# Kernel tuning notes

Hardware: AMD Instinct MI355X
Metric: run time of the kernel (lower is better)

Reference implementation:

```python
import jax, jax.numpy as jnp
import numpy as np

D_KEY = 128
INF = 1e9  # stands in for the module's global INF constant


def setup_inputs() -> dict:
    key = jax.random.key(0)
    kq, kk, kv = jax.random.split(key, 3)
    B, S, D = 8, 4096, D_KEY
    return {
        "query": jax.random.normal(kq, (B, S, D), dtype=jnp.float32),
        "keys": jax.random.normal(kk, (B, S, D), dtype=jnp.float32),
        "values": jax.random.normal(kv, (B, S, D), dtype=jnp.float32),
    }


def reference(query, keys, values):
    # dot_products: [B, Sq, Sk]
    scores = jnp.einsum("bqd,bkd->bqk", query, keys)
    S = scores.shape[-1]
    # causal: subtract INF on strict upper triangle (triu(1)), applied BEFORE scaling
    causal = jnp.triu(jnp.ones((S, S), dtype=scores.dtype), 1) * INF
    logits = (scores - causal[None, :, :]) / jnp.asarray(np.sqrt(D_KEY), scores.dtype)
    # legacy F.softmax on 3D transposed tensor == softmax over key axis
    probs = jax.nn.softmax(logits, axis=-1)
    # dropout with p=0.0 is identity
    return jnp.einsum("bqk,bkd->bqd", probs, values)
```

## Files before the change

### kernel.cpp

```cpp
#include <hip/hip_runtime.h>
#include <hip/hip_bf16.h>

#define B_SZ   8
#define S_LEN  4096
#define D_K    128
#define KB     64
#define CH     16
#define NCHUNK 1280

#define KT_STR 136
#define VT_STR 72
#define PT_STR 72

typedef short  short8  __attribute__((ext_vector_type(8)));
typedef float  floatx4 __attribute__((ext_vector_type(4)));

#define EXP2F(x) exp2f(x)

__device__ __forceinline__ unsigned bfround(float x) {
  unsigned u = __builtin_bit_cast(unsigned, x);
  return (u + 0x7fffu + ((u >> 16) & 1u)) >> 16;
}
__device__ __forceinline__ unsigned bfpack2(float a, float b) {
  return bfround(a) | (bfround(b) << 16);
}


__global__ __launch_bounds__(256)
void conv_k(const float* __restrict__ K, unsigned short* __restrict__ Kb) {
  const size_t idx = ((size_t)blockIdx.x * 256 + threadIdx.x) * 8;
  float4 f0 = *(const float4*)(K + idx);
  float4 f1 = *(const float4*)(K + idx + 4);
  uint4 u;
  u.x = bfpack2(f0.x, f0.y);
  u.y = bfpack2(f0.z, f0.w);
  u.z = bfpack2(f1.x, f1.y);
  u.w = bfpack2(f1.z, f1.w);
  *(uint4*)(Kb + idx) = u;
}

__global__ __launch_bounds__(256)
void transp_v(const float* __restrict__ V, unsigned short* __restrict__ Vt) {
  __shared__ float tile[64][65];
  const int t   = threadIdx.x;
  const int bid = blockIdx.x;
  const int b   = bid >> 7;
  const int rem = bid & 127;
  const int kt  = (rem >> 1) * 64;
  const int dt  = (rem & 1) * 64;
  {
    const int c  = (t & 15) * 4;
    const int r0 = t >> 4;
#pragma unroll
    for (int rr = 0; rr < 4; ++rr) {
      const int r = r0 + rr * 16;
      float4 f = *(const float4*)(V + (size_t)(b * S_LEN + kt + r) * D_K + dt + c);
      tile[r][c]     = f.x;
      tile[r][c + 1] = f.y;
      tile[r][c + 2] = f.z;
      tile[r][c + 3] = f.w;
    }
  }
  __syncthreads();
  {
    const int d  = t >> 2;
    const int k0 = (t & 3) * 16;
#pragma unroll
    for (int j = 0; j < 16; j += 8) {
      uint4 u;
      u.x = bfpack2(tile[k0 + j + 0][d], tile[k0 + j + 1][d]);
      u.y = bfpack2(tile[k0 + j + 2][d], tile[k0 + j + 3][d]);
      u.z = bfpack2(tile[k0 + j + 4][d], tile[k0 + j + 5][d]);
      u.w = bfpack2(tile[k0 + j + 6][d], tile[k0 + j + 7][d]);
      *(uint4*)(Vt + (size_t)(b * D_K + dt + d) * S_LEN + kt + k0 + j) = u;
    }
  }
}

__global__ void zero_cnt(int* cnt) { *cnt = 0; }


__global__ __launch_bounds__(128, 2)
void attn_worker(const float* __restrict__ Q, const unsigned short* __restrict__ Kb,
                 const unsigned short* __restrict__ Vt, int* __restrict__ cnt,
                 float* __restrict__ ml, float* __restrict__ pO) {
  __shared__ __align__(16) short Klds[KB * KT_STR];
  __shared__ __align__(16) short Vtlds[D_K * VT_STR];
  __shared__ __align__(16) short Plds[2 * 16 * PT_STR];
  __shared__ int s_chunk;

  const int tid  = threadIdx.x;
  const int lane = tid & 63;
  const int w    = tid >> 6;
  const int l15  = lane & 15;
  const int quad = lane >> 4;

  const int kr0 = tid >> 4;
  const int kc  = (tid & 15) * 8;
  const int vr0 = tid >> 3;
  const int vc  = (tid & 7) * 8;

  const float CSC = 0.12752041f;

  for (;;) {
    if (tid == 0) s_chunk = atomicAdd(cnt, 1);
    __syncthreads();
    const int c = s_chunk;
    if (c >= NCHUNK) break;

    int b, qi, j;
    if (c < 800) {
      const int r = c >> 3;  b = c & 7;
      if      (r <  4) { qi = 63;               j = r;            }
      else if (r < 52) { qi = 62 - (r-4)/3;     j = (r-4)%3;      }
      else if (r < 84) { qi = 46 - (r-52)/2;    j = (r-52)%2;     }
      else             { qi = 30 - (r-84);      j = 0;            }
    } else {
      const int rc = c - 800;
      const int s  = 15 - (rc >> 5);
      const int t  = rc & 31;
      b  = t & 7;
      qi = s - 1 + 16 * (t >> 3);
      j  = (qi + 1) >> 4;
    }

    const int q0 = qi * 64;
    const int s0 = j * CH;
    const int s1 = min(s0 + CH, qi + 1);

    short8 bq[2][4];
    int qg[2];
#pragma unroll
    for (int sub = 0; sub < 2; ++sub) {
      qg[sub] = q0 + w * 32 + sub * 16 + l15;
      const float* qrow = Q + (size_t)(b * S_LEN + qg[sub]) * D_K + quad * 8;
#pragma unroll
      for (int kd = 0; kd < 4; ++kd) {
        float4 f0 = *(const float4*)(qrow + kd * 32);
        float4 f1 = *(const float4*)(qrow + kd * 32 + 4);
        union { short8 s; unsigned u[4]; } t;
        t.u[0] = bfpack2(f0.x, f0.y);
        t.u[1] = bfpack2(f0.z, f0.w);
        t.u[2] = bfpack2(f1.x, f1.y);
        t.u[3] = bfpack2(f1.z, f1.w);
        bq[sub][kd] = t.s;
      }
    }

    floatx4 acc[2][8];
#pragma unroll
    for (int sub = 0; sub < 2; ++sub)
#pragma unroll
      for (int nc = 0; nc < 8; ++nc) acc[sub][nc] = (floatx4){0.f, 0.f, 0.f, 0.f};
    float m_run[2] = {-1e30f, -1e30f}, l_run[2] = {0.f, 0.f};

    const unsigned short* kbase = Kb + (size_t)(b * S_LEN) * D_K;
    const unsigned short* vbase = Vt + (size_t)(b * D_K) * S_LEN;

    for (int s = s0; s < s1; ++s) {
      const int kt = s * KB;

#pragma unroll
      for (int i = 0; i < 8; ++i) {
        uint4 u = *(const uint4*)(kbase + (size_t)(kt + kr0 + i * 8) * D_K + kc);
        *(uint4*)(&Klds[(kr0 + i * 8) * KT_STR + kc]) = u;
      }
#pragma unroll
      for (int i = 0; i < 8; ++i) {
        uint4 u = *(const uint4*)(vbase + (size_t)(vr0 + i * 16) * S_LEN + kt + vc);
        *(uint4*)(&Vtlds[(vr0 + i * 16) * VT_STR + vc]) = u;
      }
      __syncthreads();

      floatx4 st[2][4];
#pragma unroll
      for (int kf = 0; kf < 4; ++kf) {
        floatx4 c0 = (floatx4){0.f, 0.f, 0.f, 0.f};
        floatx4 c1 = (floatx4){0.f, 0.f, 0.f, 0.f};
#pragma unroll
        for (int kd = 0; kd < 4; ++kd) {
          short8 a = *(const short8*)(&Klds[(kf * 16 + l15) * KT_STR + kd * 32 + quad * 8]);
          c0 = __builtin_amdgcn_mfma_f32_16x16x32_bf16(a, bq[0][kd], c0, 0, 0, 0);
          c1 = __builtin_amdgcn_mfma_f32_16x16x32_bf16(a, bq[1][kd], c1, 0, 0, 0);
        }
        st[0][kf] = c0;
        st[1][kf] = c1;
      }

      if (s == qi) {
#pragma unroll
        for (int sub = 0; sub < 2; ++sub)
#pragma unroll
          for (int kf = 0; kf < 4; ++kf)
#pragma unroll
            for (int r = 0; r < 4; ++r) {
              int key = kt + kf * 16 + quad * 4 + r;
              if (key > qg[sub]) st[sub][kf][r] = -1e30f;
            }
      }

      short8 pa[2][2];
#pragma unroll
      for (int sub = 0; sub < 2; ++sub) {
        float mx = st[sub][0][0];
#pragma unroll
        for (int kf = 0; kf < 4; ++kf)
#pragma unroll
          for (int r = 0; r < 4; ++r) mx = fmaxf(mx, st[sub][kf][r]);
        mx = fmaxf(mx, __shfl_xor(mx, 16, 64));
        mx = fmaxf(mx, __shfl_xor(mx, 32, 64));
        const float m_new = fmaxf(m_run[sub], mx);
        const float alpha = EXP2F((m_run[sub] - m_new) * CSC);

        float p[4][4];
        float tsum = 0.f;
#pragma unroll
        for (int kf = 0; kf < 4; ++kf)
#pragma unroll
          for (int r = 0; r < 4; ++r) {
            p[kf][r] = EXP2F((st[sub][kf][r] - m_new) * CSC);
            tsum += p[kf][r];
          }
        tsum += __shfl_xor(tsum, 16, 64);
        tsum += __shfl_xor(tsum, 32, 64);
        l_run[sub] = l_run[sub] * alpha + tsum;
        m_run[sub] = m_new;

#pragma unroll
        for (int r = 0; r < 4; ++r) {
          const float ar = __shfl(alpha, quad * 4 + r, 64);
#pragma unroll
          for (int nc = 0; nc < 8; ++nc) acc[sub][nc][r] *= ar;
        }

        short* pw = &Plds[(w * 16 + l15) * PT_STR];
#pragma unroll
        for (int kf = 0; kf < 4; ++kf) {
          uint2 u;
          u.x = bfpack2(p[kf][0], p[kf][1]);
          u.y = bfpack2(p[kf][2], p[kf][3]);
          *(uint2*)(&pw[kf * 16 + quad * 4]) = u;
        }
        __asm__ __volatile__("" ::: "memory");
        pa[sub][0] = *(const short8*)(&pw[quad * 8]);
        pa[sub][1] = *(const short8*)(&pw[32 + quad * 8]);
        __asm__ __volatile__("" ::: "memory");
      }

#pragma unroll
      for (int nc = 0; nc < 8; ++nc) {
        short8 bv0 = *(const short8*)(&Vtlds[(nc * 16 + l15) * VT_STR + quad * 8]);
        short8 bv1 = *(const short8*)(&Vtlds[(nc * 16 + l15) * VT_STR + 32 + quad * 8]);
        acc[0][nc] = __builtin_amdgcn_mfma_f32_16x16x32_bf16(pa[0][0], bv0, acc[0][nc], 0, 0, 0);
        acc[0][nc] = __builtin_amdgcn_mfma_f32_16x16x32_bf16(pa[0][1], bv1, acc[0][nc], 0, 0, 0);
        acc[1][nc] = __builtin_amdgcn_mfma_f32_16x16x32_bf16(pa[1][0], bv0, acc[1][nc], 0, 0, 0);
        acc[1][nc] = __builtin_amdgcn_mfma_f32_16x16x32_bf16(pa[1][1], bv1, acc[1][nc], 0, 0, 0);
      }
      __syncthreads();
    }

    const int slot = ((b << 6) | qi) * 4 + j;
    float* po = pO + (size_t)slot * 8192;
#pragma unroll
    for (int sub = 0; sub < 2; ++sub) {
#pragma unroll
      for (int r = 0; r < 4; ++r) {
        const int qrow = w * 32 + sub * 16 + quad * 4 + r;
        float* op = po + qrow * D_K + l15;
#pragma unroll
        for (int nc = 0; nc < 8; ++nc) op[nc * 16] = acc[sub][nc][r];
      }
      if (quad == 0) {
        const int qrow = w * 32 + sub * 16 + l15;
        ml[(size_t)slot * 128 + qrow * 2]     = m_run[sub];
        ml[(size_t)slot * 128 + qrow * 2 + 1] = l_run[sub];
      }
    }
  }
}


__global__ __launch_bounds__(256)
void attn_combine(const float* __restrict__ ml, const float* __restrict__ pO,
                  float* __restrict__ O) {
  const int t   = blockIdx.x;
  const int b   = t >> 6;
  const int qi  = t & 63;
  const int ncb = ((qi + 1) + 15) >> 4;
  const float CSC = 0.12752041f;

  const int tid = threadIdx.x;
  const int q   = tid >> 2;
  const int dp  = (tid & 3) * 32;

  float m[4], l[4];
  float M = -1e30f;
  for (int jj = 0; jj < ncb; ++jj) {
    const int slot = t * 4 + jj;
    m[jj] = ml[(size_t)slot * 128 + q * 2];
    l[jj] = ml[(size_t)slot * 128 + q * 2 + 1];
    M = fmaxf(M, m[jj]);
  }
  float wgt[4], L = 0.f;
  for (int jj = 0; jj < ncb; ++jj) {
    wgt[jj] = EXP2F((m[jj] - M) * CSC);
    L += wgt[jj] * l[jj];
  }
  const float inv = 1.0f / L;

  float4 out[8];
#pragma unroll
  for (int v = 0; v < 8; ++v) out[v] = make_float4(0.f, 0.f, 0.f, 0.f);
  for (int jj = 0; jj < ncb; ++jj) {
    const float* src = pO + (size_t)(t * 4 + jj) * 8192 + q * D_K + dp;
    const float wj = wgt[jj];
#pragma unroll
    for (int v = 0; v < 8; ++v) {
      float4 f = *(const float4*)(src + v * 4);
      out[v].x += wj * f.x;  out[v].y += wj * f.y;
      out[v].z += wj * f.z;  out[v].w += wj * f.w;
    }
  }
  float* dst = O + (size_t)(b * S_LEN + qi * 64 + q) * D_K + dp;
#pragma unroll
  for (int v = 0; v < 8; ++v) {
    float4 f = make_float4(out[v].x * inv, out[v].y * inv, out[v].z * inv, out[v].w * inv);
    *(float4*)(dst + v * 4) = f;
  }
}


__global__ __launch_bounds__(256, 2)
void attn_fwd_fb(const float* __restrict__ Q, const float* __restrict__ K,
                 const float* __restrict__ V, float* __restrict__ O) {
  __shared__ __align__(16) short Klds[KB * KT_STR];
  __shared__ __align__(16) short Vtlds[D_K * VT_STR];
  __shared__ __align__(16) short Plds[4 * 16 * PT_STR];

  const int tid  = threadIdx.x;
  const int lane = tid & 63;
  const int w    = tid >> 6;
  const int l15  = lane & 15;
  const int quad = lane >> 4;

  const int bid = blockIdx.x;
  const int b   = bid & 7;
  const int qi  = 63 - (bid >> 3);
  const int q0  = qi * 64;

  const float CSC = 0.12752041f;

  const int    qg   = q0 + w * 16 + l15;
  const float* qrow = Q + (size_t)(b * S_LEN + qg) * D_K + quad * 8;
  short8 bq[4];
#pragma unroll
  for (int kd = 0; kd < 4; ++kd) {
    float4 f0 = *(const float4*)(qrow + kd * 32);
    float4 f1 = *(const float4*)(qrow + kd * 32 + 4);
    union { short8 s; unsigned u[4]; } t;
    t.u[0] = bfpack2(f0.x, f0.y);
    t.u[1] = bfpack2(f0.z, f0.w);
    t.u[2] = bfpack2(f1.x, f1.y);
    t.u[3] = bfpack2(f1.z, f1.w);
    bq[kd] = t.s;
  }

  floatx4 acc[8];
#pragma unroll
  for (int nc = 0; nc < 8; ++nc) acc[nc] = (floatx4){0.f, 0.f, 0.f, 0.f};
  float m_run = -1e30f, l_run = 0.f;

  const int d4 = tid & 31;
  const int kq = tid >> 5;
  const int nsteps = qi + 1;

  for (int s = 0; s < nsteps; ++s) {
    const int kt = s * KB;
#pragma unroll
    for (int r2 = 0; r2 < 2; ++r2) {
      const int row = r2 * 32 + kq * 4;
      const float* kp = K + (size_t)(b * S_LEN + kt + row) * D_K + d4 * 4;
      const float* vp = V + (size_t)(b * S_LEN + kt + row) * D_K + d4 * 4;
      float4 fk[4], fv[4];
#pragma unroll
      for (int i = 0; i < 4; ++i) {
        fk[i] = *(const float4*)(kp + i * D_K);
        fv[i] = *(const float4*)(vp + i * D_K);
      }
#pragma unroll
      for (int i = 0; i < 4; ++i) {
        uint2 u;
        u.x = bfpack2(fk[i].x, fk[i].y);
        u.y = bfpack2(fk[i].z, fk[i].w);
        *(uint2*)(&Klds[(row + i) * KT_STR + d4 * 4]) = u;
      }
#pragma unroll
      for (int c = 0; c < 4; ++c) {
        float e0 = ((const float*)&fv[0])[c];
        float e1 = ((const float*)&fv[1])[c];
        float e2 = ((const float*)&fv[2])[c];
        float e3 = ((const float*)&fv[3])[c];
        uint2 u;
        u.x = bfpack2(e0, e1);
        u.y = bfpack2(e2, e3);
        *(uint2*)(&Vtlds[(d4 * 4 + c) * VT_STR + row]) = u;
      }
    }
    __syncthreads();

    floatx4 st[4];
#pragma unroll
    for (int kf = 0; kf < 4; ++kf) {
      floatx4 c = (floatx4){0.f, 0.f, 0.f, 0.f};
#pragma unroll
      for (int kd = 0; kd < 4; ++kd) {
        short8 a = *(const short8*)(&Klds[(kf * 16 + l15) * KT_STR + kd * 32 + quad * 8]);
        c = __builtin_amdgcn_mfma_f32_16x16x32_bf16(a, bq[kd], c, 0, 0, 0);
      }
      st[kf] = c;
    }

    if (s == nsteps - 1) {
#pragma unroll
      for (int kf = 0; kf < 4; ++kf)
#pragma unroll
        for (int r = 0; r < 4; ++r) {
          int key = kt + kf * 16 + quad * 4 + r;
          if (key > qg) st[kf][r] = -1e30f;
        }
    }

    float mx = st[0][0];
#pragma unroll
    for (int kf = 0; kf < 4; ++kf)
#pragma unroll
      for (int r = 0; r < 4; ++r) mx = fmaxf(mx, st[kf][r]);
    mx = fmaxf(mx, __shfl_xor(mx, 16, 64));
    mx = fmaxf(mx, __shfl_xor(mx, 32, 64));
    const float m_new = fmaxf(m_run, mx);
    const float alpha = EXP2F((m_run - m_new) * CSC);

    float p[4][4];
    float tsum = 0.f;
#pragma unroll
    for (int kf = 0; kf < 4; ++kf)
#pragma unroll
      for (int r = 0; r < 4; ++r) {
        p[kf][r] = EXP2F((st[kf][r] - m_new) * CSC);
        tsum += p[kf][r];
      }
    tsum += __shfl_xor(tsum, 16, 64);
    tsum += __shfl_xor(tsum, 32, 64);
    l_run = l_run * alpha + tsum;
    m_run = m_new;

#pragma unroll
    for (int r = 0; r < 4; ++r) {
      const float ar = __shfl(alpha, quad * 4 + r, 64);
#pragma unroll
      for (int nc = 0; nc < 8; ++nc) acc[nc][r] *= ar;
    }

    short* pw = &Plds[(w * 16 + l15) * PT_STR];
#pragma unroll
    for (int kf = 0; kf < 4; ++kf) {
      uint2 u;
      u.x = bfpack2(p[kf][0], p[kf][1]);
      u.y = bfpack2(p[kf][2], p[kf][3]);
      *(uint2*)(&pw[kf * 16 + quad * 4]) = u;
    }
    __asm__ __volatile__("" ::: "memory");
    short8 pa0 = *(const short8*)(&pw[quad * 8]);
    short8 pa1 = *(const short8*)(&pw[32 + quad * 8]);

#pragma unroll
    for (int nc = 0; nc < 8; ++nc) {
      short8 bv0 = *(const short8*)(&Vtlds[(nc * 16 + l15) * VT_STR + quad * 8]);
      acc[nc] = __builtin_amdgcn_mfma_f32_16x16x32_bf16(pa0, bv0, acc[nc], 0, 0, 0);
      short8 bv1 = *(const short8*)(&Vtlds[(nc * 16 + l15) * VT_STR + 32 + quad * 8]);
      acc[nc] = __builtin_amdgcn_mfma_f32_16x16x32_bf16(pa1, bv1, acc[nc], 0, 0, 0);
    }
    __syncthreads();
  }

#pragma unroll
  for (int r = 0; r < 4; ++r) {
    const float lr  = __shfl(l_run, quad * 4 + r, 64);
    const float inv = 1.0f / lr;
    const int qout  = q0 + w * 16 + quad * 4 + r;
    float* op = O + (size_t)(b * S_LEN + qout) * D_K + l15;
#pragma unroll
    for (int nc = 0; nc < 8; ++nc) op[nc * 16] = acc[nc][r] * inv;
  }
}


extern "C" void kernel_launch(void* const* d_in, const int* in_sizes, int n_in,
                              void* d_out, int out_size, void* d_ws, size_t ws_size,
                              hipStream_t stream) {
  const float* Q = (const float*)d_in[0];
  const float* K = (const float*)d_in[1];
  const float* V = (const float*)d_in[2];
  float* O = (float*)d_out;

  const size_t elems = (size_t)B_SZ * S_LEN * D_K;

  const size_t off_ml = 256;
  const size_t off_po = off_ml + 2048ull * 128 * 4;
  const size_t off_kb = off_po + 2048ull * 8192 * 4;
  const size_t off_vt = off_kb + elems * 2;
  const size_t need   = off_vt + elems * 2;

  if (ws_size >= need) {
    char* ws = (char*)d_ws;
    int*            cnt = (int*)ws;
    float*          ml  = (float*)(ws + off_ml);
    float*          po  = (float*)(ws + off_po);
    unsigned short* Kb  = (unsigned short*)(ws + off_kb);
    unsigned short* Vt  = (unsigned short*)(ws + off_vt);

    zero_cnt<<<dim3(1), dim3(1), 0, stream>>>(cnt);
    conv_k<<<dim3((unsigned)(elems / 8 / 256)), dim3(256), 0, stream>>>(K, Kb);
    transp_v<<<dim3(B_SZ * (S_LEN / 64) * (D_K / 64)), dim3(256), 0, stream>>>(V, Vt);
    attn_worker<<<dim3(1024), dim3(128), 0, stream>>>(Q, Kb, Vt, cnt, ml, po);
    attn_combine<<<dim3(512), dim3(256), 0, stream>>>(ml, po, O);
  } else {
    attn_fwd_fb<<<dim3(512), dim3(256), 0, stream>>>(Q, K, V, O);
  }
}
```

Before: 195.3 us.

## Double-buffer K/V tiles via async global-to-LDS DMA with pre-swizzled tile layout

Merges the K conversion and V transpose into one prep kernel that writes each 64-key tile as a contiguous 8192-element block, with an XOR swizzle matching the LDS read pattern. The attention worker now double-buffers K and V tiles in LDS using global_load_lds DMA, prefetching tile s+2 while tile s is computed. This is meant to hide global-load latency and avoid bank conflicts without padded strides. P packing also switches to the hardware v_cvt_pk_bf16_f32 instruction. The cost is doubled LDS use, which may limit occupancy, plus hand-managed waitcnt/barrier ordering that is fragile.

After: 217.7 us. 1.11x slower.

```diff
diff --git a/kernel.cpp b/kernel.cpp
--- a/kernel.cpp
+++ b/kernel.cpp
@@ -1,5 +1,4 @@
 #include <hip/hip_runtime.h>
-#include <hip/hip_bf16.h>
 
 #define B_SZ   8
 #define S_LEN  4096
@@ -8,8 +7,6 @@
 #define CH     16
 #define NCHUNK 1280
 
-#define KT_STR 136
-#define VT_STR 72
 #define PT_STR 72
 
 typedef short  short8  __attribute__((ext_vector_type(8)));
@@ -24,55 +21,80 @@
 __device__ __forceinline__ unsigned bfpack2(float a, float b) {
   return bfround(a) | (bfround(b) << 16);
 }
+__device__ __forceinline__ unsigned cvtpk(float lo, float hi) {
+  unsigned r;
+  asm("v_cvt_pk_bf16_f32 %0, %1, %2" : "=v"(r) : "v"(lo), "v"(hi));
+  return r;
+}
+
+__device__ __forceinline__ void dma16(const void* g, const void* l) {
+  __builtin_amdgcn_global_load_lds(
+      (__attribute__((address_space(1))) unsigned int*)(unsigned long long)g,
+      (__attribute__((address_space(3))) unsigned int*)(unsigned int)(unsigned long long)l,
+      16, 0, 0);
+}
 
 
 __global__ __launch_bounds__(256)
-void conv_k(const float* __restrict__ K, unsigned short* __restrict__ Kb) {
-  const size_t idx = ((size_t)blockIdx.x * 256 + threadIdx.x) * 8;
-  float4 f0 = *(const float4*)(K + idx);
-  float4 f1 = *(const float4*)(K + idx + 4);
-  uint4 u;
-  u.x = bfpack2(f0.x, f0.y);
-  u.y = bfpack2(f0.z, f0.w);
-  u.z = bfpack2(f1.x, f1.y);
-  u.w = bfpack2(f1.z, f1.w);
-  *(uint4*)(Kb + idx) = u;
-}
-
-__global__ __launch_bounds__(256)
-void transp_v(const float* __restrict__ V, unsigned short* __restrict__ Vt) {
-  __shared__ float tile[64][65];
-  const int t   = threadIdx.x;
+void prep(const float* __restrict__ K, const float* __restrict__ V,
+          unsigned short* __restrict__ Kb, unsigned short* __restrict__ Vt) {
+  __shared__ float tile[64][129];
+  const int tid = threadIdx.x;
   const int bid = blockIdx.x;
-  const int b   = bid >> 7;
-  const int rem = bid & 127;
-  const int kt  = (rem >> 1) * 64;
-  const int dt  = (rem & 1) * 64;
+  const int b   = bid >> 6;
+  const int s   = bid & 63;
+  const int kt  = s * 64;
+
   {
-    const int c  = (t & 15) * 4;
-    const int r0 = t >> 4;
-#pragma unroll
-    for (int rr = 0; rr < 4; ++rr) {
-      const int r = r0 + rr * 16;
-      float4 f = *(const float4*)(V + (size_t)(b * S_LEN + kt + r) * D_K + dt + c);
-      tile[r][c]     = f.x;
-      tile[r][c + 1] = f.y;
-      tile[r][c + 2] = f.z;
-      tile[r][c + 3] = f.w;
+    const int r  = tid >> 2;
+    const int cq = tid & 3;
+    const float* kp = K + (size_t)(b * S_LEN + kt + r) * D_K + cq * 32;
+    unsigned short* kdst = Kb + (size_t)bid * 8192 + r * 128;
+    const int xr = (r & 7) << 4;
+#pragma unroll
+    for (int j = 0; j < 4; ++j) {
+      float4 f0 = *(const float4*)(kp + j * 8);
+      float4 f1 = *(const float4*)(kp + j * 8 + 4);
+      uint4 u;
+      u.x = bfpack2(f0.x, f0.y);
+      u.y = bfpack2(f0.z, f0.w);
+      u.z = bfpack2(f1.x, f1.y);
+      u.w = bfpack2(f1.z, f1.w);
+      const int o = (cq * 64 + j * 16) ^ xr;
+      *(uint4*)(kdst + (o >> 1)) = u;
+    }
+  }
+
+  {
+    const int k  = tid >> 2;
+    const int cq = tid & 3;
+    const float* vp = V + (size_t)(b * S_LEN + kt + k) * D_K + cq * 32;
+#pragma unroll
+    for (int i = 0; i < 8; ++i) {
+      float4 f = *(const float4*)(vp + i * 4);
+      tile[k][cq * 32 + i * 4]     = f.x;
+      tile[k][cq * 32 + i * 4 + 1] = f.y;
+      tile[k][cq * 32 + i * 4 + 2] = f.z;
+      tile[k][cq * 32 + i * 4 + 3] = f.w;
     }
   }
   __syncthreads();
+
   {
-    const int d  = t >> 2;
-    const int k0 = (t & 3) * 16;
-#pragma unroll
-    for (int j = 0; j < 16; j += 8) {
+    const int d = tid >> 1;
+    const int h = tid & 1;
+    unsigned short* vdst = Vt + (size_t)bid * 8192 + d * 64;
+    const int xr = (d & 7) << 4;
+#pragma unroll
+    for (int j = 0; j < 4; ++j) {
+      const int k0 = h * 32 + j * 8;
       uint4 u;
-      u.x = bfpack2(tile[k0 + j + 0][d], tile[k0 + j + 1][d]);
-      u.y = bfpack2(tile[k0 + j + 2][d], tile[k0 + j + 3][d]);
-      u.z = bfpack2(tile[k0 + j + 4][d], tile[k0 + j + 5][d]);
-      u.w = bfpack2(tile[k0 + j + 6][d], tile[k0 + j + 7][d]);
-      *(uint4*)(Vt + (size_t)(b * D_K + dt + d) * S_LEN + kt + k0 + j) = u;
+      u.x = bfpack2(tile[k0 + 0][d], tile[k0 + 1][d]);
+      u.y = bfpack2(tile[k0 + 2][d], tile[k0 + 3][d]);
+      u.z = bfpack2(tile[k0 + 4][d], tile[k0 + 5][d]);
+      u.w = bfpack2(tile[k0 + 6][d], tile[k0 + 7][d]);
+      const int o = (h * 64 + j * 16) ^ xr;
+      *(uint4*)(vdst + (o >> 1)) = u;
     }
   }
 }
@@ -84,8 +106,8 @@
 void attn_worker(const float* __restrict__ Q, const unsigned short* __restrict__ Kb,
                  const unsigned short* __restrict__ Vt, int* __restrict__ cnt,
                  float* __restrict__ ml, float* __restrict__ pO) {
-  __shared__ __align__(16) short Klds[KB * KT_STR];
-  __shared__ __align__(16) short Vtlds[D_K * VT_STR];
+  __shared__ __align__(16) short Klds[2][8192];
+  __shared__ __align__(16) short Vtlds[2][8192];
   __shared__ __align__(16) short Plds[2 * 16 * PT_STR];
   __shared__ int s_chunk;
 
@@ -94,11 +116,7 @@
   const int w    = tid >> 6;
   const int l15  = lane & 15;
   const int quad = lane >> 4;
-
-  const int kr0 = tid >> 4;
-  const int kc  = (tid & 15) * 8;
-  const int vr0 = tid >> 3;
-  const int vc  = (tid & 7) * 8;
+  const int xk   = (l15 & 7) << 3;
 
   const float CSC = 0.12752041f;
 
@@ -154,23 +172,37 @@
       for (int nc = 0; nc < 8; ++nc) acc[sub][nc] = (floatx4){0.f, 0.f, 0.f, 0.f};
     float m_run[2] = {-1e30f, -1e30f}, l_run[2] = {0.f, 0.f};
 
-    const unsigned short* kbase = Kb + (size_t)(b * S_LEN) * D_K;
-    const unsigned short* vbase = Vt + (size_t)(b * D_K) * S_LEN;
+    const unsigned short* kb0 = Kb + (size_t)b * 64 * 8192;
+    const unsigned short* vb0 = Vt + (size_t)b * 64 * 8192;
+    const int lo = lane * 8;
+
+#define STAGE(BUF, S)                                                          \
+    do {                                                                       \
+      const unsigned short* kg_ = kb0 + (size_t)(S) * 8192 + w * 4096 + lo;    \
+      const unsigned short* vg_ = vb0 + (size_t)(S) * 8192 + w * 4096 + lo;    \
+      short* kl_ = &Klds[BUF][w * 4096];                                       \
+      short* vl_ = &Vtlds[BUF][w * 4096];                                      \
+      _Pragma("unroll")                                                        \
+      for (int i_ = 0; i_ < 8; ++i_) dma16(kg_ + i_ * 512, kl_ + i_ * 512);    \
+      _Pragma("unroll")                                                        \
+      for (int i_ = 0; i_ < 8; ++i_) dma16(vg_ + i_ * 512, vl_ + i_ * 512);    \
+    } while (0)
+
+    STAGE(s0 & 1, s0);
+    if (s0 + 1 < s1) {
+      STAGE((s0 + 1) & 1, s0 + 1);
+      asm volatile("s_waitcnt vmcnt(16)" ::: "memory");
+    } else {
+      asm volatile("s_waitcnt vmcnt(0)" ::: "memory");
+    }
+    __builtin_amdgcn_s_barrier();
+    __builtin_amdgcn_sched_barrier(0);
 
     for (int s = s0; s < s1; ++s) {
-      const int kt = s * KB;
-
-#pragma unroll
-      for (int i = 0; i < 8; ++i) {
-        uint4 u = *(const uint4*)(kbase + (size_t)(kt + kr0 + i * 8) * D_K + kc);
-        *(uint4*)(&Klds[(kr0 + i * 8) * KT_STR + kc]) = u;
-      }
-#pragma unroll
-      for (int i = 0; i < 8; ++i) {
-        uint4 u = *(const uint4*)(vbase + (size_t)(vr0 + i * 16) * S_LEN + kt + vc);
-        *(uint4*)(&Vtlds[(vr0 + i * 16) * VT_STR + vc]) = u;
-      }
-      __syncthreads();
+      const int kt  = s * KB;
+      const int cur = s & 1;
+      const short* Kl = &Klds[cur][0];
+      const short* Vl = &Vtlds[cur][0];
 
       floatx4 st[2][4];
 #pragma unroll
@@ -179,7 +211,7 @@
         floatx4 c1 = (floatx4){0.f, 0.f, 0.f, 0.f};
 #pragma unroll
         for (int kd = 0; kd < 4; ++kd) {
-          short8 a = *(const short8*)(&Klds[(kf * 16 + l15) * KT_STR + kd * 32 + quad * 8]);
+          short8 a = *(const short8*)(&Kl[((kf * 16 + l15) << 7) + ((kd * 32 + quad * 8) ^ xk)]);
           c0 = __builtin_amdgcn_mfma_f32_16x16x32_bf16(a, bq[0][kd], c0, 0, 0, 0);
           c1 = __builtin_amdgcn_mfma_f32_16x16x32_bf16(a, bq[1][kd], c1, 0, 0, 0);
         }
@@ -237,8 +269,8 @@
 #pragma unroll
         for (int kf = 0; kf < 4; ++kf) {
           uint2 u;
-          u.x = bfpack2(p[kf][0], p[kf][1]);
-          u.y = bfpack2(p[kf][2], p[kf][3]);
+          u.x = cvtpk(p[kf][0], p[kf][1]);
+          u.y = cvtpk(p[kf][2], p[kf][3]);
           *(uint2*)(&pw[kf * 16 + quad * 4]) = u;
         }
         __asm__ __volatile__("" ::: "memory");
@@ -249,15 +281,27 @@
 
 #pragma unroll
       for (int nc = 0; nc < 8; ++nc) {
-        short8 bv0 = *(const short8*)(&Vtlds[(nc * 16 + l15) * VT_STR + quad * 8]);
-        short8 bv1 = *(const short8*)(&Vtlds[(nc * 16 + l15) * VT_STR + 32 + quad * 8]);
+        short8 bv0 = *(const short8*)(&Vl[((nc * 16 + l15) << 6) + ((quad * 8) ^ xk)]);
+        short8 bv1 = *(const short8*)(&Vl[((nc * 16 + l15) << 6) + ((32 + quad * 8) ^ xk)]);
         acc[0][nc] = __builtin_amdgcn_mfma_f32_16x16x32_bf16(pa[0][0], bv0, acc[0][nc], 0, 0, 0);
         acc[0][nc] = __builtin_amdgcn_mfma_f32_16x16x32_bf16(pa[0][1], bv1, acc[0][nc], 0, 0, 0);
         acc[1][nc] = __builtin_amdgcn_mfma_f32_16x16x32_bf16(pa[1][0], bv0, acc[1][nc], 0, 0, 0);
         acc[1][nc] = __builtin_amdgcn_mfma_f32_16x16x32_bf16(pa[1][1], bv1, acc[1][nc], 0, 0, 0);
       }
-      __syncthreads();
-    }
+
+      asm volatile("s_waitcnt lgkmcnt(0)" ::: "memory");
+      __builtin_amdgcn_s_barrier();
+      __builtin_amdgcn_sched_barrier(0);
+      if (s + 2 < s1) {
+        STAGE(cur, s + 2);
+        asm volatile("s_waitcnt vmcnt(16)" ::: "memory");
+      } else if (s + 1 < s1) {
+        asm volatile("s_waitcnt vmcnt(0)" ::: "memory");
+      }
+      __builtin_amdgcn_s_barrier();
+      __builtin_amdgcn_sched_barrier(0);
+    }
+#undef STAGE
 
     const int slot = ((b << 6) | qi) * 4 + j;
     float* po = pO + (size_t)slot * 8192;
@@ -329,6 +373,9 @@
   }
 }
 
+
+#define KT_STR 136
+#define VT_STR 72
 
 __global__ __launch_bounds__(256, 2)
 void attn_fwd_fb(const float* __restrict__ Q, const float* __restrict__ K,
@@ -424,9 +471,9 @@
 #pragma unroll
       for (int kf = 0; kf < 4; ++kf)
 #pragma unroll
-        for (int r = 0; r < 4; ++r) {
-          int key = kt + kf * 16 + quad * 4 + r;
-          if (key > qg) st[kf][r] = -1e30f;
+        for (int rr = 0; rr < 4; ++rr) {
+          int key = kt + kf * 16 + quad * 4 + rr;
+          if (key > qg) st[kf][rr] = -1e30f;
         }
     }
 
@@ -434,7 +481,7 @@
 #pragma unroll
     for (int kf = 0; kf < 4; ++kf)
 #pragma unroll
-      for (int r = 0; r < 4; ++r) mx = fmaxf(mx, st[kf][r]);
+      for (int rr = 0; rr < 4; ++rr) mx = fmaxf(mx, st[kf][rr]);
     mx = fmaxf(mx, __shfl_xor(mx, 16, 64));
     mx = fmaxf(mx, __shfl_xor(mx, 32, 64));
     const float m_new = fmaxf(m_run, mx);
@@ -445,9 +492,9 @@
 #pragma unroll
     for (int kf = 0; kf < 4; ++kf)
 #pragma unroll
-      for (int r = 0; r < 4; ++r) {
-        p[kf][r] = EXP2F((st[kf][r] - m_new) * CSC);
-        tsum += p[kf][r];
+      for (int rr = 0; rr < 4; ++rr) {
+        p[kf][rr] = EXP2F((st[kf][rr] - m_new) * CSC);
+        tsum += p[kf][rr];
       }
     tsum += __shfl_xor(tsum, 16, 64);
     tsum += __shfl_xor(tsum, 32, 64);
@@ -455,10 +502,10 @@
     m_run = m_new;
 
 #pragma unroll
-    for (int r = 0; r < 4; ++r) {
-      const float ar = __shfl(alpha, quad * 4 + r, 64);
-#pragma unroll
-      for (int nc = 0; nc < 8; ++nc) acc[nc][r] *= ar;
+    for (int rr = 0; rr < 4; ++rr) {
+      const float ar = __shfl(alpha, quad * 4 + rr, 64);
+#pragma unroll
+      for (int nc = 0; nc < 8; ++nc) acc[nc][rr] *= ar;
     }
 
     short* pw = &Plds[(w * 16 + l15) * PT_STR];
@@ -484,13 +531,13 @@
   }
 
 #pragma unroll
-  for (int r = 0; r < 4; ++r) {
-    const float lr  = __shfl(l_run, quad * 4 + r, 64);
+  for (int rr = 0; rr < 4; ++rr) {
+    const float lr  = __shfl(l_run, quad * 4 + rr, 64);
     const float inv = 1.0f / lr;
-    const int qout  = q0 + w * 16 + quad * 4 + r;
+    const int qout  = q0 + w * 16 + quad * 4 + rr;
     float* op = O + (size_t)(b * S_LEN + qout) * D_K + l15;
 #pragma unroll
-    for (int nc = 0; nc < 8; ++nc) op[nc * 16] = acc[nc][r] * inv;
+    for (int nc = 0; nc < 8; ++nc) op[nc * 16] = acc[nc][rr] * inv;
   }
 }
 
@@ -514,16 +561,15 @@
   if (ws_size >= need) {
     char* ws = (char*)d_ws;
     int*            cnt = (int*)ws;
-    float*          ml  = (float*)(ws + off_ml);
+    float*          mlp = (float*)(ws + off_ml);
     float*          po  = (float*)(ws + off_po);
-    unsigned short* Kb  = (unsigned short*)(ws + off_kb);
-    unsigned short* Vt  = (unsigned short*)(ws + off_vt);
+    unsigned short* Kbp = (unsigned short*)(ws + off_kb);
+    unsigned short* Vtp = (unsigned short*)(ws + off_vt);
 
     zero_cnt<<<dim3(1), dim3(1), 0, stream>>>(cnt);
-    conv_k<<<dim3((unsigned)(elems / 8 / 256)), dim3(256), 0, stream>>>(K, Kb);
-    transp_v<<<dim3(B_SZ * (S_LEN / 64) * (D_K / 64)), dim3(256), 0, stream>>>(V, Vt);
-    attn_worker<<<dim3(1024), dim3(128), 0, stream>>>(Q, Kb, Vt, cnt, ml, po);
-    attn_combine<<<dim3(512), dim3(256), 0, stream>>>(ml, po, O);
+    prep<<<dim3(B_SZ * 64), dim3(256), 0, stream>>>(K, V, Kbp, Vtp);
+    attn_worker<<<dim3(1024), dim3(128), 0, stream>>>(Q, Kbp, Vtp, cnt, mlp, po);
+    attn_combine<<<dim3(512), dim3(256), 0, stream>>>(mlp, po, O);
   } else {
     attn_fwd_fb<<<dim3(512), dim3(256), 0, stream>>>(Q, K, V, O);
   }
```
